# Performance work log

Measured on AMD Instinct MI355X. Metric: run time of the kernel, lower is better.

The kernel has to match this reference:

```python
import jax, jax.numpy as jnp
import numpy as np
from jax import lax

D = 1024      # hidden_dim
H = 1408      # moe_inter_dim
E = 8         # num_experts
K = 2         # topk
ROUTER_SCALE = 1.0


def setup_inputs() -> dict:
    key = jax.random.key(0)
    ks = jax.random.split(key, 16)
    s = 0.02
    inp = {
        "x": jax.random.normal(ks[0], (2, 2048, D), dtype=jnp.float32),
        "gate_w": jax.random.normal(ks[1], (E, D), dtype=jnp.float32) * s,
        "gate_b": jax.random.normal(ks[2], (E,), dtype=jnp.float32) * s,
        # stacked expert params; torch Linear weight [out,in] stored transposed as [in,out]
        "w1": jax.random.normal(ks[3], (E, D, H), dtype=jnp.float32) * s,
        "b1": jax.random.normal(ks[4], (E, H), dtype=jnp.float32) * s,
        "w3": jax.random.normal(ks[5], (E, D, H), dtype=jnp.float32) * s,
        "b3": jax.random.normal(ks[6], (E, H), dtype=jnp.float32) * s,
        "w2": jax.random.normal(ks[7], (E, H, D), dtype=jnp.float32) * s,
        "b2": jax.random.normal(ks[8], (E, D), dtype=jnp.float32) * s,
        # shared expert
        "sw1": jax.random.normal(ks[9], (D, H), dtype=jnp.float32) * s,
        "sb1": jax.random.normal(ks[10], (H,), dtype=jnp.float32) * s,
        "sw3": jax.random.normal(ks[11], (D, H), dtype=jnp.float32) * s,
        "sb3": jax.random.normal(ks[12], (H,), dtype=jnp.float32) * s,
        "sw2": jax.random.normal(ks[13], (H, D), dtype=jnp.float32) * s,
        "sb2": jax.random.normal(ks[14], (D,), dtype=jnp.float32) * s,
    }
    return inp


def _expert(x, w1, b1, w3, b3, w2, b2):
    # NOTE: source applies silu to the PRODUCT: w2(silu(w1(x) * w3(x)))
    h = jax.nn.silu((x @ w1 + b1) * (x @ w3 + b3))
    return h @ w2 + b2


def reference(x, gate_w, gate_b, w1, b1, w3, b3, w2, b2,
              sw1, sb1, sw3, sb3, sw2, sb2):
    shape = x.shape
    xf = x.reshape(-1, D)                      # [T, D]
    T = xf.shape[0]

    # Gate
    scores = jax.nn.softmax(xf @ gate_w.T, axis=-1)   # [T, E]
    biased = scores + gate_b
    _, idx = lax.top_k(biased, K)                     # [T, K] int32
    w = jnp.take_along_axis(scores, idx, axis=-1) * ROUTER_SCALE  # [T, K]

    # Dense routing-weight matrix (top-k indices are distinct per token)
    rw = jnp.zeros((T, E), dtype=xf.dtype).at[jnp.arange(T)[:, None], idx].add(w)

    # Stacked expert compute: [T, E, H] -> [T, E, D], combined by routing weight
    h = jax.nn.silu((jnp.einsum('td,edh->teh', xf, w1) + b1)
                    * (jnp.einsum('td,edh->teh', xf, w3) + b3))
    oe = jnp.einsum('teh,ehd->ted', h, w2) + b2
    y = jnp.einsum('te,ted->td', rw, oe)

    # Shared expert on all tokens
    z = _expert(xf, sw1, sb1, sw3, sb3, sw2, sb2)
    return (y + z).reshape(shape)
```

## Files before the change

### kernel.cpp

```cpp
#include <hip/hip_runtime.h>
#include <math.h>

#define DD 1024
#define HH 1408
#define NE 8

typedef __attribute__((ext_vector_type(8))) __bf16 bf16x8;
typedef __attribute__((ext_vector_type(4))) float f32x4;

__device__ __forceinline__ float bf2f(unsigned short u) {
  union { unsigned int i; float f; } v; v.i = ((unsigned int)u) << 16; return v.f;
}
__device__ __forceinline__ unsigned short f2bf(float f) {
  union { float f; unsigned int i; } v; v.f = f;
  unsigned int r = v.i + 0x7FFFu + ((v.i >> 16) & 1u);
  return (unsigned short)(r >> 16);
}
__device__ __forceinline__ float tof(float f) { return f; }
__device__ __forceinline__ float tof(unsigned short u) { return bf2f(u); }

__device__ __forceinline__ void cvt2(float a, float b, unsigned int* o) {
  asm("v_cvt_pk_bf16_f32 %0, %1, %2" : "=v"(*o) : "v"(a), "v"(b));
}

__device__ __forceinline__ void ld8cvt(const float* p, unsigned int* o) {
  float4 a = *(const float4*)p;
  float4 b = *(const float4*)(p + 4);
  cvt2(a.x, a.y, o + 0); cvt2(a.z, a.w, o + 1);
  cvt2(b.x, b.y, o + 2); cvt2(b.z, b.w, o + 3);
}

__global__ void sniff_kernel(const unsigned short* __restrict__ xw,
                             int* __restrict__ dflag) {
  __shared__ int cnt;
  if (threadIdx.x == 0) cnt = 0;
  __syncthreads();
  unsigned short v = xw[threadIdx.x];
  int e = (v >> 7) & 0xFF;
  if (e >= 100 && e <= 140) atomicAdd(&cnt, 1);
  __syncthreads();
  if (threadIdx.x == 0) dflag[0] = (cnt < 230) ? 1 : 0;
}

__global__ void cvtx_kernel(const void* __restrict__ x,
                            const int* __restrict__ dflag,
                            unsigned short* __restrict__ xb, int n8) {
  int i = blockIdx.x * blockDim.x + threadIdx.x;
  int st = gridDim.x * blockDim.x;
  if (dflag[0]) {
    const float* xs = (const float*)x;
    for (; i < n8; i += st) {
      unsigned int o[4];
      ld8cvt(xs + (size_t)i * 8, o);
      *(uint4*)(xb + (size_t)i * 8) = *(uint4*)o;
    }
  } else {
    const uint4* xs = (const uint4*)x;
    for (; i < n8; i += st) *(uint4*)(xb + (size_t)i * 8) = xs[i];
  }
}

__global__ void trans_kernel(const void* __restrict__ wmain,
                             const void* __restrict__ wsh,
                             const int* __restrict__ dflag,
                             unsigned short* __restrict__ out, int R, int C) {
  __shared__ float tile[32][33];
  const int mat = blockIdx.z;
  const int r0 = blockIdx.y << 5, c0 = blockIdx.x << 5;
  const int t = threadIdx.x;
  const int lr = t >> 3, lc = (t & 7) << 2;
  const size_t mbase = (size_t)mat * R * C;
  if (dflag[0]) {
    const float* src = (mat < NE) ? ((const float*)wmain + mbase) : (const float*)wsh;
    float4 v = *(const float4*)(src + (size_t)(r0 + lr) * C + c0 + lc);
    tile[lr][lc] = v.x; tile[lr][lc + 1] = v.y;
    tile[lr][lc + 2] = v.z; tile[lr][lc + 3] = v.w;
  } else {
    const unsigned short* src = (mat < NE) ? ((const unsigned short*)wmain + mbase)
                                           : (const unsigned short*)wsh;
    ushort4 v = *(const ushort4*)(src + (size_t)(r0 + lr) * C + c0 + lc);
    tile[lr][lc] = bf2f(v.x); tile[lr][lc + 1] = bf2f(v.y);
    tile[lr][lc + 2] = bf2f(v.z); tile[lr][lc + 3] = bf2f(v.w);
  }
  __syncthreads();
  const int oc = t >> 3;
  const int orr = (t & 7) << 2;
  unsigned int p0, p1;
  cvt2(tile[orr][oc], tile[orr + 1][oc], &p0);
  cvt2(tile[orr + 2][oc], tile[orr + 3][oc], &p1);
  uint2 pk; pk.x = p0; pk.y = p1;
  *(uint2*)(out + mbase + (size_t)(c0 + oc) * R + r0 + orr) = pk;
}

__global__ void cvtb_kernel(const void* b1, const void* b3, const void* b2,
                            const void* sb1, const void* sb3, const void* sb2,
                            const int* __restrict__ dflag,
                            float* __restrict__ bf1, float* __restrict__ bf3,
                            float* __restrict__ bf2o) {
  int i = blockIdx.x * blockDim.x + threadIdx.x;
  const int nh = (NE + 1) * HH, nd = (NE + 1) * DD;
  const bool f32 = dflag[0] != 0;
  auto get = [&](const void* pm, const void* ps, int idx, int per) -> float {
    int mat = idx / per, j = idx - mat * per;
    if (f32) return (mat < NE) ? ((const float*)pm)[(size_t)mat * per + j]
                               : ((const float*)ps)[j];
    return bf2f((mat < NE) ? ((const unsigned short*)pm)[(size_t)mat * per + j]
                           : ((const unsigned short*)ps)[j]);
  };
  if (i < nh) bf1[i] = get(b1, sb1, i, HH);
  else if (i < 2 * nh) bf3[i - nh] = get(b3, sb3, i - nh, HH);
  else if (i < 2 * nh + nd) bf2o[i - 2 * nh] = get(b2, sb2, i - 2 * nh, DD);
}

template <class T>
__device__ void gate_body(const T* __restrict__ x,
                          const T* __restrict__ gw,
                          const T* __restrict__ gb,
                          int* __restrict__ tok_eidx,
                          float* __restrict__ tok_w, int T_) {
  int t = (int)((blockIdx.x * blockDim.x + threadIdx.x) >> 6);
  int lane = threadIdx.x & 63;
  if (t >= T_) return;
  const T* xr = x + (size_t)t * DD;
  float acc[NE];
#pragma unroll
  for (int e = 0; e < NE; e++) acc[e] = 0.f;
  for (int i = lane; i < DD; i += 64) {
    float xv = tof(xr[i]);
#pragma unroll
    for (int e = 0; e < NE; e++) acc[e] += xv * tof(gw[e * DD + i]);
  }
#pragma unroll
  for (int off = 32; off > 0; off >>= 1) {
#pragma unroll
    for (int e = 0; e < NE; e++) acc[e] += __shfl_xor(acc[e], off);
  }
  if (lane == 0) {
    float mx = acc[0];
#pragma unroll
    for (int e = 1; e < NE; e++) mx = fmaxf(mx, acc[e]);
    float s = 0.f, sc[NE], bi[NE];
#pragma unroll
    for (int e = 0; e < NE; e++) { sc[e] = expf(acc[e] - mx); s += sc[e]; }
    float inv = 1.f / s;
#pragma unroll
    for (int e = 0; e < NE; e++) { sc[e] *= inv; bi[e] = sc[e] + tof(gb[e]); }
    int i1 = 0;
#pragma unroll
    for (int e = 1; e < NE; e++) if (bi[e] > bi[i1]) i1 = e;
    int i2 = (i1 == 0) ? 1 : 0;
#pragma unroll
    for (int e = 0; e < NE; e++) if (e != i1 && bi[e] > bi[i2]) i2 = e;
    tok_eidx[t * 2] = i1; tok_eidx[t * 2 + 1] = i2;
    tok_w[t * 2] = sc[i1]; tok_w[t * 2 + 1] = sc[i2];
  }
}

__global__ void gate_kernel(const void* x, const void* gw, const void* gb,
                            const int* __restrict__ dflag,
                            int* tok_eidx, float* tok_w, int T_) {
  if (dflag[0])
    gate_body<float>((const float*)x, (const float*)gw, (const float*)gb,
                     tok_eidx, tok_w, T_);
  else
    gate_body<unsigned short>((const unsigned short*)x, (const unsigned short*)gw,
                              (const unsigned short*)gb, tok_eidx, tok_w, T_);
}

__global__ void prep_kernel(const int* __restrict__ tok_eidx,
                            const float* __restrict__ tok_w,
                            int* __restrict__ meta,
                            int* __restrict__ rows_tok,
                            float* __restrict__ rows_wgt,
                            int t0, int TS) {
  __shared__ int cnt[NE];
  __shared__ int off[NE];
  const int tid = threadIdx.x;
  if (tid < NE) cnt[tid] = 0;
  __syncthreads();
  const int n2 = TS * 2;
  const int* te = tok_eidx + (size_t)t0 * 2;
  const float* tw = tok_w + (size_t)t0 * 2;
  for (int i = tid; i < n2; i += (int)blockDim.x) atomicAdd(&cnt[te[i]], 1);
  __syncthreads();
  if (tid == 0) {
    int s = 0;
#pragma unroll
    for (int e = 0; e < NE; e++) { off[e] = s; meta[16 + e] = s; s += cnt[e]; }
    meta[16 + NE] = s;
  }
  __syncthreads();
  for (int i = tid; i < n2; i += (int)blockDim.x) {
    int pos = atomicAdd(&off[te[i]], 1);
    rows_tok[pos] = t0 + (i >> 1);
    rows_wgt[pos] = tw[i];
  }
}

__global__ void zero_kernel(float4* __restrict__ p, int n4) {
  int i = blockIdx.x * blockDim.x + threadIdx.x;
  int st = gridDim.x * blockDim.x;
  float4 z; z.x = z.y = z.z = z.w = 0.f;
  for (; i < n4; i += st) p[i] = z;
}

__global__ __launch_bounds__(512, 4)
void ffn_up_kernel(const unsigned short* __restrict__ xb,
                   const unsigned short* __restrict__ wt1,
                   const unsigned short* __restrict__ wt3,
                   const float* __restrict__ bf1, const float* __restrict__ bf3,
                   const int* __restrict__ meta,
                   const int* __restrict__ rows_tok,
                   unsigned short* __restrict__ h_buf,
                   unsigned short* __restrict__ sh_buf,
                   int t0, int TS) {
  const int z = blockIdx.z;
  const bool shx = (z == NE);
  int g0, cnt;
  unsigned short* ho;
  if (shx) { g0 = 0; cnt = TS; ho = sh_buf; }
  else {
    g0 = meta[16 + z]; cnt = meta[17 + z] - g0;
    ho = h_buf + (size_t)g0 * HH;
  }
  const int mtile = blockIdx.y;
  if (mtile * 128 >= cnt) return;
  const int n0 = blockIdx.x * 128;
  const unsigned short* wa = wt1 + (size_t)z * HH * DD;
  const unsigned short* wb = wt3 + (size_t)z * HH * DD;

  __shared__ alignas(16) unsigned short lds_a[128 * 40];
  __shared__ alignas(16) unsigned short lds_b1[128 * 40];
  __shared__ alignas(16) unsigned short lds_b3[128 * 40];

  const int tid = threadIdx.x;
  const int row = tid >> 2, cc = (tid & 3) << 3;
  int m = mtile * 128 + row;
  int srow;
  if (shx) srow = t0 + ((m < cnt) ? m : (cnt - 1));
  else { int r = (m < cnt) ? m : (cnt - 1); srow = rows_tok[g0 + r]; }
  const size_t abase = (size_t)srow * DD + cc;
  const size_t bbase = (size_t)(n0 + row) * DD + cc;
  const int soff = row * 40 + cc;

  const int wid = tid >> 6;
  const int wrow = (wid >> 1) << 5;
  const int wcol = (wid & 1) << 6;
  const int ln15 = tid & 15;
  const int kq8 = ((tid & 63) >> 4) << 3;

  f32x4 acc1[2][4], acc3[2][4];
#pragma unroll
  for (int a = 0; a < 2; a++)
#pragma unroll
    for (int b = 0; b < 4; b++) {
      acc1[a][b] = {0.f, 0.f, 0.f, 0.f};
      acc3[a][b] = {0.f, 0.f, 0.f, 0.f};
    }

  for (int k0 = 0; k0 < DD; k0 += 32) {
    __syncthreads();
    *(uint4*)&lds_a[soff]  = *(const uint4*)(xb + abase + k0);
    *(uint4*)&lds_b1[soff] = *(const uint4*)(wa + bbase + k0);
    *(uint4*)&lds_b3[soff] = *(const uint4*)(wb + bbase + k0);
    __syncthreads();
    bf16x8 af[2];
#pragma unroll
    for (int fm = 0; fm < 2; fm++)
      af[fm] = *(const bf16x8*)&lds_a[(wrow + fm * 16 + ln15) * 40 + kq8];
#pragma unroll
    for (int fn = 0; fn < 4; fn++) {
      bf16x8 bv1 = *(const bf16x8*)&lds_b1[(wcol + fn * 16 + ln15) * 40 + kq8];
      bf16x8 bv3 = *(const bf16x8*)&lds_b3[(wcol + fn * 16 + ln15) * 40 + kq8];
#pragma unroll
      for (int fm = 0; fm < 2; fm++) {
        acc1[fm][fn] = __builtin_amdgcn_mfma_f32_16x16x32_bf16(af[fm], bv1, acc1[fm][fn], 0, 0, 0);
        acc3[fm][fn] = __builtin_amdgcn_mfma_f32_16x16x32_bf16(af[fm], bv3, acc3[fm][fn], 0, 0, 0);
      }
    }
  }

  const int kq4 = ((tid & 63) >> 4) << 2;
#pragma unroll
  for (int fm = 0; fm < 2; fm++) {
#pragma unroll
    for (int r = 0; r < 4; r++) {
      int mm = mtile * 128 + wrow + fm * 16 + kq4 + r;
      if (mm < cnt) {
        unsigned short* orow = ho + (size_t)mm * HH + n0;
#pragma unroll
        for (int fn = 0; fn < 4; fn++) {
          int nc = wcol + fn * 16 + ln15;
          float g1 = acc1[fm][fn][r] + bf1[(size_t)z * HH + n0 + nc];
          float g3 = acc3[fm][fn][r] + bf3[(size_t)z * HH + n0 + nc];
          float u = g1 * g3;
          float hv = u * __builtin_amdgcn_rcpf(1.f + __expf(-u));
          orow[nc] = f2bf(hv);
        }
      }
    }
  }
}

__global__ __launch_bounds__(512, 4)
void ffn_down_kernel(const unsigned short* __restrict__ h_buf,
                     const unsigned short* __restrict__ sh_buf,
                     const unsigned short* __restrict__ wt2,
                     const float* __restrict__ bf2,
                     const int* __restrict__ meta,
                     const int* __restrict__ rows_tok,
                     const float* __restrict__ rows_wgt,
                     float* __restrict__ out, int t0, int TS) {
  const int z = blockIdx.z;
  const bool shx = (z == NE);
  int g0, cnt;
  const unsigned short* hb;
  if (shx) { g0 = 0; cnt = TS; hb = sh_buf; }
  else {
    g0 = meta[16 + z]; cnt = meta[17 + z] - g0;
    hb = h_buf + (size_t)g0 * HH;
  }
  const int mtile = blockIdx.y;
  if (mtile * 128 >= cnt) return;
  const int n0 = blockIdx.x * 128;
  const unsigned short* wsrc = wt2 + (size_t)z * DD * HH;

  __shared__ alignas(16) unsigned short lds_a[128 * 40];
  __shared__ alignas(16) unsigned short lds_b[128 * 40];

  const int tid = threadIdx.x;
  const int row = tid >> 2, cc = (tid & 3) << 3;
  int m = mtile * 128 + row;
  int r = (m < cnt) ? m : (cnt - 1);
  const unsigned short* asrc = hb + (size_t)r * HH + cc;
  const size_t bbase = (size_t)(n0 + row) * HH + cc;
  const int soff = row * 40 + cc;

  const int wid = tid >> 6;
  const int wrow = (wid >> 1) << 5;
  const int wcol = (wid & 1) << 6;
  const int ln15 = tid & 15;
  const int kq8 = ((tid & 63) >> 4) << 3;

  f32x4 acc[2][4];
#pragma unroll
  for (int a = 0; a < 2; a++)
#pragma unroll
    for (int b = 0; b < 4; b++) acc[a][b] = {0.f, 0.f, 0.f, 0.f};

  for (int k0 = 0; k0 < HH; k0 += 32) {
    __syncthreads();
    *(uint4*)&lds_a[soff] = *(const uint4*)(asrc + k0);
    *(uint4*)&lds_b[soff] = *(const uint4*)(wsrc + bbase + k0);
    __syncthreads();
    bf16x8 af[2];
#pragma unroll
    for (int fm = 0; fm < 2; fm++)
      af[fm] = *(const bf16x8*)&lds_a[(wrow + fm * 16 + ln15) * 40 + kq8];
#pragma unroll
    for (int fn = 0; fn < 4; fn++) {
      bf16x8 bv = *(const bf16x8*)&lds_b[(wcol + fn * 16 + ln15) * 40 + kq8];
#pragma unroll
      for (int fm = 0; fm < 2; fm++)
        acc[fm][fn] = __builtin_amdgcn_mfma_f32_16x16x32_bf16(af[fm], bv, acc[fm][fn], 0, 0, 0);
    }
  }

  const int kq4 = ((tid & 63) >> 4) << 2;
#pragma unroll
  for (int fm = 0; fm < 2; fm++) {
#pragma unroll
    for (int r4 = 0; r4 < 4; r4++) {
      int mm = mtile * 128 + wrow + fm * 16 + kq4 + r4;
      if (mm < cnt) {
        int t; float wgt;
        if (shx) { t = t0 + mm; wgt = 1.f; }
        else { t = rows_tok[g0 + mm]; wgt = rows_wgt[g0 + mm]; }
        float* orow = out + (size_t)t * DD + n0;
#pragma unroll
        for (int fn = 0; fn < 4; fn++) {
          int nc = wcol + fn * 16 + ln15;
          float v = wgt * (acc[fm][fn][r4] + bf2[(size_t)z * DD + n0 + nc]);
          atomicAdd(&orow[nc], v);
        }
      }
    }
  }
}

extern "C" void kernel_launch(void* const* d_in, const int* in_sizes, int n_in,
                              void* d_out, int out_size, void* d_ws, size_t ws_size,
                              hipStream_t stream) {
  const void* x   = d_in[0];
  const void* gw  = d_in[1];
  const void* gb  = d_in[2];
  const void* w1  = d_in[3];
  const void* b1  = d_in[4];
  const void* w3  = d_in[5];
  const void* b3  = d_in[6];
  const void* w2  = d_in[7];
  const void* b2  = d_in[8];
  const void* sw1 = d_in[9];
  const void* sb1 = d_in[10];
  const void* sw3 = d_in[11];
  const void* sb3 = d_in[12];
  const void* sw2 = d_in[13];
  const void* sb2 = d_in[14];

  const int T = in_sizes[0] / DD;
  (void)n_in; (void)out_size;

  const size_t WMAT = (size_t)(NE + 1) * HH * DD;

  auto need = [&](int S) -> size_t {
    int TS = T / S;
    size_t o = 0;
    auto pad = [&](size_t b) { o = (o + b + 255) & ~(size_t)255; };
    pad(256);
    pad(32 * sizeof(int));
    pad((size_t)T * 2 * sizeof(int));
    pad((size_t)T * 2 * sizeof(float));
    pad((size_t)T * DD * 2);
    pad(WMAT * 2);
    pad(WMAT * 2);
    pad(WMAT * 2);
    pad((size_t)(NE + 1) * HH * sizeof(float));
    pad((size_t)(NE + 1) * HH * sizeof(float));
    pad((size_t)(NE + 1) * DD * sizeof(float));
    pad((size_t)TS * 2 * sizeof(int));
    pad((size_t)TS * 2 * sizeof(float));
    pad((size_t)TS * 2 * HH * 2);
    pad((size_t)TS * HH * 2);
    return o;
  };
  int S = 32;
  {
    const int cand[6] = {1, 2, 4, 8, 16, 32};
    for (int ci = 0; ci < 6; ci++) {
      if (need(cand[ci]) <= ws_size) { S = cand[ci]; break; }
    }
  }
  const int TS = T / S;
  const int mt = TS / 128;

  char* w = (char*)d_ws;
  size_t off = 0;
  auto take = [&](size_t bytes) {
    char* p = w + off;
    off = (off + bytes + 255) & ~(size_t)255;
    return p;
  };
  int*   dflag    = (int*)  take(256);
  int*   meta     = (int*)  take(32 * sizeof(int));
  int*   tok_eidx = (int*)  take((size_t)T * 2 * sizeof(int));
  float* tok_w    = (float*)take((size_t)T * 2 * sizeof(float));
  unsigned short* xb  = (unsigned short*)take((size_t)T * DD * 2);
  unsigned short* wt1 = (unsigned short*)take(WMAT * 2);
  unsigned short* wt3 = (unsigned short*)take(WMAT * 2);
  unsigned short* wt2 = (unsigned short*)take(WMAT * 2);
  float* bf1 = (float*)take((size_t)(NE + 1) * HH * sizeof(float));
  float* bf3 = (float*)take((size_t)(NE + 1) * HH * sizeof(float));
  float* bf2 = (float*)take((size_t)(NE + 1) * DD * sizeof(float));
  int*   rows_tok = (int*)  take((size_t)TS * 2 * sizeof(int));
  float* rows_wgt = (float*)take((size_t)TS * 2 * sizeof(float));
  unsigned short* h_buf  = (unsigned short*)take((size_t)TS * 2 * HH * 2);
  unsigned short* sh_buf = (unsigned short*)take((size_t)TS * HH * 2);

  sniff_kernel<<<1, 256, 0, stream>>>((const unsigned short*)x, dflag);

  cvtx_kernel<<<2048, 256, 0, stream>>>(x, dflag, xb, T * DD / 8);
  trans_kernel<<<dim3(HH / 32, DD / 32, NE + 1), 256, 0, stream>>>(w1, sw1, dflag, wt1, DD, HH);
  trans_kernel<<<dim3(HH / 32, DD / 32, NE + 1), 256, 0, stream>>>(w3, sw3, dflag, wt3, DD, HH);
  trans_kernel<<<dim3(DD / 32, HH / 32, NE + 1), 256, 0, stream>>>(w2, sw2, dflag, wt2, HH, DD);
  {
    int nb = (2 * (NE + 1) * HH + (NE + 1) * DD + 255) / 256;
    cvtb_kernel<<<nb, 256, 0, stream>>>(b1, b3, b2, sb1, sb3, sb2, dflag, bf1, bf3, bf2);
  }

  gate_kernel<<<(T + 3) / 4, 256, 0, stream>>>(x, gw, gb, dflag, tok_eidx, tok_w, T);
  zero_kernel<<<1024, 256, 0, stream>>>((float4*)d_out, T * DD / 4);

  for (int s = 0; s < S; s++) {
    const int t0 = s * TS;
    prep_kernel<<<1, 1024, 0, stream>>>(tok_eidx, tok_w, meta, rows_tok, rows_wgt, t0, TS);
    ffn_up_kernel<<<dim3(HH / 128, mt, NE + 1), 512, 0, stream>>>(
        xb, wt1, wt3, bf1, bf3, meta, rows_tok, h_buf, sh_buf, t0, TS);
    ffn_down_kernel<<<dim3(DD / 128, mt, NE + 1), 512, 0, stream>>>(
        h_buf, sh_buf, wt2, bf2, meta, rows_tok, rows_wgt, (float*)d_out, t0, TS);
  }
}
```

Before: 502.4 us.

## Double-buffer FFN GEMMs with direct global-to-LDS loads and larger 256-row tiles

Rewrites the up and down FFN GEMM kernels to use 256x128 output tiles with a 64-wide K step, double-buffered LDS staging through global_load_lds, and an XOR-swizzled LDS layout in place of the padded rows. The aim is to overlap the next tile's global loads with the current tile's MFMAs, raise arithmetic intensity per block, and avoid LDS bank conflicts. In exchange, accumulator registers and LDS use grow, so occupancy drops to 2 blocks per CU, and the coarser M tiles can waste more work on small expert groups and give fewer blocks per launch.

```diff
diff --git a/kernel.cpp b/kernel.cpp
--- a/kernel.cpp
+++ b/kernel.cpp
@@ -28,6 +28,12 @@
   float4 b = *(const float4*)(p + 4);
   cvt2(a.x, a.y, o + 0); cvt2(a.z, a.w, o + 1);
   cvt2(b.x, b.y, o + 2); cvt2(b.z, b.w, o + 3);
+}
+
+typedef unsigned int __attribute__((address_space(1))) gu32;
+typedef unsigned int __attribute__((address_space(3))) lu32;
+__device__ __forceinline__ void gl16(const unsigned short* g, unsigned short* l) {
+  __builtin_amdgcn_global_load_lds((const gu32*)g, (lu32*)l, 16, 0, 0);
 }
 
 __global__ void sniff_kernel(const unsigned short* __restrict__ xw,
@@ -204,7 +210,7 @@
   for (; i < n4; i += st) p[i] = z;
 }
 
-__global__ __launch_bounds__(512, 4)
+__global__ __launch_bounds__(512, 2)
 void ffn_up_kernel(const unsigned short* __restrict__ xb,
                    const unsigned short* __restrict__ wt1,
                    const unsigned short* __restrict__ wt3,
@@ -224,73 +230,100 @@
     ho = h_buf + (size_t)g0 * HH;
   }
   const int mtile = blockIdx.y;
-  if (mtile * 128 >= cnt) return;
+  if (mtile * 256 >= cnt) return;
   const int n0 = blockIdx.x * 128;
   const unsigned short* wa = wt1 + (size_t)z * HH * DD;
   const unsigned short* wb = wt3 + (size_t)z * HH * DD;
 
-  __shared__ alignas(16) unsigned short lds_a[128 * 40];
-  __shared__ alignas(16) unsigned short lds_b1[128 * 40];
-  __shared__ alignas(16) unsigned short lds_b3[128 * 40];
+  __shared__ alignas(16) unsigned short lds[2 * 32768];
 
   const int tid = threadIdx.x;
-  const int row = tid >> 2, cc = (tid & 3) << 3;
-  int m = mtile * 128 + row;
-  int srow;
-  if (shx) srow = t0 + ((m < cnt) ? m : (cnt - 1));
-  else { int r = (m < cnt) ? m : (cnt - 1); srow = rows_tok[g0 + r]; }
-  const size_t abase = (size_t)srow * DD + cc;
-  const size_t bbase = (size_t)(n0 + row) * DD + cc;
-  const int soff = row * 40 + cc;
-
-  const int wid = tid >> 6;
-  const int wrow = (wid >> 1) << 5;
-  const int wcol = (wid & 1) << 6;
-  const int ln15 = tid & 15;
-  const int kq8 = ((tid & 63) >> 4) << 3;
-
-  f32x4 acc1[2][4], acc3[2][4];
-#pragma unroll
-  for (int a = 0; a < 2; a++)
+  const int lane = tid & 63, wid = tid >> 6;
+  const int rsub = wid * 8 + (lane >> 3);
+  const int sl8 = (((lane & 7) ^ (lane >> 3)) << 3);
+
+  size_t aoff[4];
+#pragma unroll
+  for (int c = 0; c < 4; c++) {
+    int r = c * 64 + rsub;
+    int m = mtile * 256 + r;
+    int rr = (m < cnt) ? m : (cnt - 1);
+    int srow = shx ? (t0 + rr) : rows_tok[g0 + rr];
+    aoff[c] = (size_t)srow * DD + sl8;
+  }
+  size_t boff[2];
+#pragma unroll
+  for (int c = 0; c < 2; c++)
+    boff[c] = (size_t)(n0 + c * 64 + rsub) * DD + sl8;
+
+  const int ln15 = lane & 15;
+  const int lg = lane >> 4;
+  const int wr = (wid >> 1) << 6;
+  const int wc = (wid & 1) << 6;
+  const int ldsw = wid * 512;
+
+  f32x4 acc1[4][4], acc3[4][4];
+#pragma unroll
+  for (int a = 0; a < 4; a++)
 #pragma unroll
     for (int b = 0; b < 4; b++) {
       acc1[a][b] = {0.f, 0.f, 0.f, 0.f};
       acc3[a][b] = {0.f, 0.f, 0.f, 0.f};
     }
 
-  for (int k0 = 0; k0 < DD; k0 += 32) {
+  auto stage = [&](int buf, int k) {
+    unsigned short* Lb = &lds[buf * 32768];
+#pragma unroll
+    for (int c = 0; c < 4; c++)
+      gl16(xb + aoff[c] + k, Lb + c * 4096 + ldsw);
+#pragma unroll
+    for (int c = 0; c < 2; c++) {
+      gl16(wa + boff[c] + k, Lb + 16384 + c * 4096 + ldsw);
+      gl16(wb + boff[c] + k, Lb + 24576 + c * 4096 + ldsw);
+    }
+  };
+
+  stage(0, 0);
+  const int NT = DD / 64;
+  for (int t = 0; t < NT; ++t) {
+    asm volatile("s_waitcnt vmcnt(0)" ::: "memory");
     __syncthreads();
-    *(uint4*)&lds_a[soff]  = *(const uint4*)(xb + abase + k0);
-    *(uint4*)&lds_b1[soff] = *(const uint4*)(wa + bbase + k0);
-    *(uint4*)&lds_b3[soff] = *(const uint4*)(wb + bbase + k0);
-    __syncthreads();
-    bf16x8 af[2];
-#pragma unroll
-    for (int fm = 0; fm < 2; fm++)
-      af[fm] = *(const bf16x8*)&lds_a[(wrow + fm * 16 + ln15) * 40 + kq8];
-#pragma unroll
-    for (int fn = 0; fn < 4; fn++) {
-      bf16x8 bv1 = *(const bf16x8*)&lds_b1[(wcol + fn * 16 + ln15) * 40 + kq8];
-      bf16x8 bv3 = *(const bf16x8*)&lds_b3[(wcol + fn * 16 + ln15) * 40 + kq8];
-#pragma unroll
-      for (int fm = 0; fm < 2; fm++) {
-        acc1[fm][fn] = __builtin_amdgcn_mfma_f32_16x16x32_bf16(af[fm], bv1, acc1[fm][fn], 0, 0, 0);
-        acc3[fm][fn] = __builtin_amdgcn_mfma_f32_16x16x32_bf16(af[fm], bv3, acc3[fm][fn], 0, 0, 0);
+    if (t + 1 < NT) stage((t + 1) & 1, (t + 1) * 64);
+    const unsigned short* Lb = &lds[(t & 1) * 32768];
+#pragma unroll
+    for (int ks = 0; ks < 2; ks++) {
+      bf16x8 af[4];
+#pragma unroll
+      for (int fm = 0; fm < 4; fm++) {
+        int R = wr + fm * 16 + ln15;
+        af[fm] = *(const bf16x8*)&Lb[R * 64 + ((((ks << 2) | lg) ^ (R & 7)) << 3)];
       }
-    }
-  }
-
-  const int kq4 = ((tid & 63) >> 4) << 2;
-#pragma unroll
-  for (int fm = 0; fm < 2; fm++) {
+#pragma unroll
+      for (int fn = 0; fn < 4; fn++) {
+        int Rb = wc + fn * 16 + ln15;
+        int o = Rb * 64 + ((((ks << 2) | lg) ^ (Rb & 7)) << 3);
+        bf16x8 b1v = *(const bf16x8*)&Lb[16384 + o];
+        bf16x8 b3v = *(const bf16x8*)&Lb[24576 + o];
+#pragma unroll
+        for (int fm = 0; fm < 4; fm++) {
+          acc1[fm][fn] = __builtin_amdgcn_mfma_f32_16x16x32_bf16(af[fm], b1v, acc1[fm][fn], 0, 0, 0);
+          acc3[fm][fn] = __builtin_amdgcn_mfma_f32_16x16x32_bf16(af[fm], b3v, acc3[fm][fn], 0, 0, 0);
+        }
+      }
+    }
+  }
+
+  const int kq4 = lg << 2;
+#pragma unroll
+  for (int fm = 0; fm < 4; fm++) {
 #pragma unroll
     for (int r = 0; r < 4; r++) {
-      int mm = mtile * 128 + wrow + fm * 16 + kq4 + r;
-      if (mm < cnt) {
-        unsigned short* orow = ho + (size_t)mm * HH + n0;
+      int m = mtile * 256 + wr + fm * 16 + kq4 + r;
+      if (m < cnt) {
+        unsigned short* orow = ho + (size_t)m * HH + n0;
 #pragma unroll
         for (int fn = 0; fn < 4; fn++) {
-          int nc = wcol + fn * 16 + ln15;
+          int nc = wc + fn * 16 + ln15;
           float g1 = acc1[fm][fn][r] + bf1[(size_t)z * HH + n0 + nc];
           float g3 = acc3[fm][fn][r] + bf3[(size_t)z * HH + n0 + nc];
           float u = g1 * g3;
@@ -302,7 +335,7 @@
   }
 }
 
-__global__ __launch_bounds__(512, 4)
+__global__ __launch_bounds__(512, 2)
 void ffn_down_kernel(const unsigned short* __restrict__ h_buf,
                      const unsigned short* __restrict__ sh_buf,
                      const unsigned short* __restrict__ wt2,
@@ -321,65 +354,93 @@
     hb = h_buf + (size_t)g0 * HH;
   }
   const int mtile = blockIdx.y;
-  if (mtile * 128 >= cnt) return;
+  if (mtile * 256 >= cnt) return;
   const int n0 = blockIdx.x * 128;
-  const unsigned short* wsrc = wt2 + (size_t)z * DD * HH;
-
-  __shared__ alignas(16) unsigned short lds_a[128 * 40];
-  __shared__ alignas(16) unsigned short lds_b[128 * 40];
+  const unsigned short* ws = wt2 + (size_t)z * DD * HH;
+
+  __shared__ alignas(16) unsigned short lds[2 * 24576];
 
   const int tid = threadIdx.x;
-  const int row = tid >> 2, cc = (tid & 3) << 3;
-  int m = mtile * 128 + row;
-  int r = (m < cnt) ? m : (cnt - 1);
-  const unsigned short* asrc = hb + (size_t)r * HH + cc;
-  const size_t bbase = (size_t)(n0 + row) * HH + cc;
-  const int soff = row * 40 + cc;
-
-  const int wid = tid >> 6;
-  const int wrow = (wid >> 1) << 5;
-  const int wcol = (wid & 1) << 6;
-  const int ln15 = tid & 15;
-  const int kq8 = ((tid & 63) >> 4) << 3;
-
-  f32x4 acc[2][4];
-#pragma unroll
-  for (int a = 0; a < 2; a++)
+  const int lane = tid & 63, wid = tid >> 6;
+  const int rsub = wid * 8 + (lane >> 3);
+  const int sl8 = (((lane & 7) ^ (lane >> 3)) << 3);
+
+  size_t aoff[4];
+#pragma unroll
+  for (int c = 0; c < 4; c++) {
+    int r = c * 64 + rsub;
+    int m = mtile * 256 + r;
+    int rr = (m < cnt) ? m : (cnt - 1);
+    aoff[c] = (size_t)rr * HH + sl8;
+  }
+  size_t boff[2];
+#pragma unroll
+  for (int c = 0; c < 2; c++)
+    boff[c] = (size_t)(n0 + c * 64 + rsub) * HH + sl8;
+
+  const int ln15 = lane & 15;
+  const int lg = lane >> 4;
+  const int wr = (wid >> 1) << 6;
+  const int wc = (wid & 1) << 6;
+  const int ldsw = wid * 512;
+
+  f32x4 acc[4][4];
+#pragma unroll
+  for (int a = 0; a < 4; a++)
 #pragma unroll
     for (int b = 0; b < 4; b++) acc[a][b] = {0.f, 0.f, 0.f, 0.f};
 
-  for (int k0 = 0; k0 < HH; k0 += 32) {
+  auto stage = [&](int buf, int k) {
+    unsigned short* Lb = &lds[buf * 24576];
+#pragma unroll
+    for (int c = 0; c < 4; c++)
+      gl16(hb + aoff[c] + k, Lb + c * 4096 + ldsw);
+#pragma unroll
+    for (int c = 0; c < 2; c++)
+      gl16(ws + boff[c] + k, Lb + 16384 + c * 4096 + ldsw);
+  };
+
+  stage(0, 0);
+  const int NT = HH / 64;
+  for (int t = 0; t < NT; ++t) {
+    asm volatile("s_waitcnt vmcnt(0)" ::: "memory");
     __syncthreads();
-    *(uint4*)&lds_a[soff] = *(const uint4*)(asrc + k0);
-    *(uint4*)&lds_b[soff] = *(const uint4*)(wsrc + bbase + k0);
-    __syncthreads();
-    bf16x8 af[2];
-#pragma unroll
-    for (int fm = 0; fm < 2; fm++)
-      af[fm] = *(const bf16x8*)&lds_a[(wrow + fm * 16 + ln15) * 40 + kq8];
-#pragma unroll
-    for (int fn = 0; fn < 4; fn++) {
-      bf16x8 bv = *(const bf16x8*)&lds_b[(wcol + fn * 16 + ln15) * 40 + kq8];
-#pragma unroll
-      for (int fm = 0; fm < 2; fm++)
-        acc[fm][fn] = __builtin_amdgcn_mfma_f32_16x16x32_bf16(af[fm], bv, acc[fm][fn], 0, 0, 0);
-    }
-  }
-
-  const int kq4 = ((tid & 63) >> 4) << 2;
-#pragma unroll
-  for (int fm = 0; fm < 2; fm++) {
+    if (t + 1 < NT) stage((t + 1) & 1, (t + 1) * 64);
+    const unsigned short* Lb = &lds[(t & 1) * 24576];
+#pragma unroll
+    for (int ks = 0; ks < 2; ks++) {
+      bf16x8 af[4];
+#pragma unroll
+      for (int fm = 0; fm < 4; fm++) {
+        int R = wr + fm * 16 + ln15;
+        af[fm] = *(const bf16x8*)&Lb[R * 64 + ((((ks << 2) | lg) ^ (R & 7)) << 3)];
+      }
+#pragma unroll
+      for (int fn = 0; fn < 4; fn++) {
+        int Rb = wc + fn * 16 + ln15;
+        int o = Rb * 64 + ((((ks << 2) | lg) ^ (Rb & 7)) << 3);
+        bf16x8 bv = *(const bf16x8*)&Lb[16384 + o];
+#pragma unroll
+        for (int fm = 0; fm < 4; fm++)
+          acc[fm][fn] = __builtin_amdgcn_mfma_f32_16x16x32_bf16(af[fm], bv, acc[fm][fn], 0, 0, 0);
+      }
+    }
+  }
+
+  const int kq4 = lg << 2;
+#pragma unroll
+  for (int fm = 0; fm < 4; fm++) {
 #pragma unroll
     for (int r4 = 0; r4 < 4; r4++) {
-      int mm = mtile * 128 + wrow + fm * 16 + kq4 + r4;
-      if (mm < cnt) {
+      int m = mtile * 256 + wr + fm * 16 + kq4 + r4;
+      if (m < cnt) {
         int t; float wgt;
-        if (shx) { t = t0 + mm; wgt = 1.f; }
-        else { t = rows_tok[g0 + mm]; wgt = rows_wgt[g0 + mm]; }
+        if (shx) { t = t0 + m; wgt = 1.f; }
+        else { t = rows_tok[g0 + m]; wgt = rows_wgt[g0 + m]; }
         float* orow = out + (size_t)t * DD + n0;
 #pragma unroll
         for (int fn = 0; fn < 4; fn++) {
-          int nc = wcol + fn * 16 + ln15;
+          int nc = wc + fn * 16 + ln15;
           float v = wgt * (acc[fm][fn][r4] + bf2[(size_t)z * DD + n0 + nc]);
           atomicAdd(&orow[nc], v);
         }
@@ -441,7 +502,7 @@
     }
   }
   const int TS = T / S;
-  const int mt = TS / 128;
+  const int my = (TS + 255) / 256;
 
   char* w = (char*)d_ws;
   size_t off = 0;
@@ -483,9 +544,9 @@
   for (int s = 0; s < S; s++) {
     const int t0 = s * TS;
     prep_kernel<<<1, 1024, 0, stream>>>(tok_eidx, tok_w, meta, rows_tok, rows_wgt, t0, TS);
-    ffn_up_kernel<<<dim3(HH / 128, mt, NE + 1), 512, 0, stream>>>(
+    ffn_up_kernel<<<dim3(HH / 128, my, NE + 1), 512, 0, stream>>>(
         xb, wt1, wt3, bf1, bf3, meta, rows_tok, h_buf, sh_buf, t0, TS);
-    ffn_down_kernel<<<dim3(DD / 128, mt, NE + 1), 512, 0, stream>>>(
+    ffn_down_kernel<<<dim3(DD / 128, my, NE + 1), 512, 0, stream>>>(
         h_buf, sh_buf, wt2, bf2, meta, rows_tok, rows_wgt, (float*)d_out, t0, TS);
   }
 }
```

After: 438.3 us. -12.8%, faster.
